# Kernel tuning notes

Hardware: AMD Instinct MI355X
Metric: run time of the kernel (lower is better)

## Reference

```python
import jax, jax.numpy as jnp
import numpy as np

B, S, D, F, E, TOP_K = 4, 2048, 1024, 4096, 8, 2


def setup_inputs() -> dict:
    key = jax.random.key(0)
    ks = jax.random.split(key, 6)
    sd = 1.0 / np.sqrt(D)
    sf = 1.0 / np.sqrt(F)
    return {
        "x": jax.random.normal(ks[0], (B, S, D), dtype=jnp.float32),
        "router_w": jax.random.normal(ks[1], (E, D), dtype=jnp.float32) * sd,
        "router_b": jnp.zeros((E,), dtype=jnp.float32),
        "w1": jax.random.normal(ks[2], (E, F, D), dtype=jnp.float32) * sd,  # Linear(d_model->d_ff) weight [out,in]
        "w2": jax.random.normal(ks[3], (E, D, F), dtype=jnp.float32) * sf,  # Linear(d_ff->d_model)
        "w3": jax.random.normal(ks[4], (E, F, D), dtype=jnp.float32) * sd,
    }


def reference(x, router_w, router_b, w1, w2, w3):
    # Router: softmax over experts, then top-k with renormalized gates.
    logits = jnp.einsum("bsd,ed->bse", x, router_w) + router_b          # [B,S,E]
    probs = jax.nn.softmax(logits, axis=-1)
    topk_p, topk_i = jax.lax.top_k(probs, TOP_K)                         # [B,S,K]
    topk_p = topk_p / jnp.sum(topk_p, axis=-1, keepdims=True)
    # Per-token combine weight for each expert (0 if not selected).
    combine = jnp.sum(jax.nn.one_hot(topk_i, E, dtype=x.dtype) * topk_p[..., None], axis=-2)  # [B,S,E]

    # Note: expert(x*mask)*mask == expert(x)*mask since SwiGLU(0)=0 (no bias).
    out = jnp.zeros_like(x)
    for e in range(E):  # small fixed expert count
        h = jax.nn.silu(jnp.einsum("bsd,fd->bsf", x, w1[e])) * jnp.einsum("bsd,fd->bsf", x, w3[e])
        out = out + combine[..., e:e + 1] * jnp.einsum("bsf,df->bsd", h, w2[e])
    return out
```

## Files before the change

kernel.cpp:

```cpp
#include <hip/hip_runtime.h>
#include <hip/hip_fp16.h>


#define NTOK 8192
#define D_ 1024
#define F_ 4096
#define E_ 8
#define SLOT_CAP 18432

using half8 = __attribute__((ext_vector_type(8))) _Float16;
using half4 = __attribute__((ext_vector_type(4))) _Float16;
using f32x4 = __attribute__((ext_vector_type(4))) float;

__device__ __forceinline__ void gload16(const void* g, void* l) {
  __builtin_amdgcn_global_load_lds((const __attribute__((address_space(1))) void*)g,
                                   (__attribute__((address_space(3))) void*)l, 16, 0, 0);
}

__global__ __launch_bounds__(256) void cvt_kernel(const float* __restrict__ src,
                                                  _Float16* __restrict__ dst, int n4) {
  int i = blockIdx.x * 256 + threadIdx.x;
  int stride = gridDim.x * 256;
  for (; i < n4; i += stride) {
    float4 v = ((const float4*)src)[i];
    half4 h;
    h.x = (_Float16)v.x; h.y = (_Float16)v.y; h.z = (_Float16)v.z; h.w = (_Float16)v.w;
    ((half4*)dst)[i] = h;
  }
}

__global__ __launch_bounds__(256) void cvt_w13_kernel(const float* __restrict__ w1,
                                                      const float* __restrict__ w3,
                                                      _Float16* __restrict__ w13, int n4) {
  int i = blockIdx.x * 256 + threadIdx.x;
  int stride = gridDim.x * 256;
  for (; i < n4; i += stride) {
    int d4 = i & 255;
    int row = i >> 8;
    int e = row >> 12, f = row & 4095;
    size_t vbase = ((size_t)e << 13) | ((size_t)(f >> 4) << 5) | (size_t)(f & 15);
    float4 v1 = ((const float4*)w1)[i];
    float4 v3 = ((const float4*)w3)[i];
    half4 h1, h3;
    h1.x = (_Float16)v1.x; h1.y = (_Float16)v1.y; h1.z = (_Float16)v1.z; h1.w = (_Float16)v1.w;
    h3.x = (_Float16)v3.x; h3.y = (_Float16)v3.y; h3.z = (_Float16)v3.z; h3.w = (_Float16)v3.w;
    ((half4*)w13)[vbase * 256 + d4] = h1;
    ((half4*)w13)[(vbase + 16) * 256 + d4] = h3;
  }
}

__global__ __launch_bounds__(256) void router_kernel(
    const float* __restrict__ x, const float* __restrict__ rw, const float* __restrict__ rbias,
    _Float16* __restrict__ x16, int* __restrict__ tok_e, float* __restrict__ tok_g,
    int* __restrict__ counts) {
  int wv = threadIdx.x >> 6, lane = threadIdx.x & 63;
  int t = blockIdx.x * 4 + wv;
  const float4* xr = (const float4*)(x + (size_t)t * D_);
  float acc[E_];
#pragma unroll
  for (int e = 0; e < E_; ++e) acc[e] = 0.f;
  for (int i = lane; i < D_ / 4; i += 64) {
    float4 xv = xr[i];
    half4 hx;
    hx.x = (_Float16)xv.x; hx.y = (_Float16)xv.y; hx.z = (_Float16)xv.z; hx.w = (_Float16)xv.w;
    ((half4*)(x16 + (size_t)t * D_))[i] = hx;
#pragma unroll
    for (int e = 0; e < E_; ++e) {
      float4 wv4 = ((const float4*)(rw + (size_t)e * D_))[i];
      acc[e] += xv.x * wv4.x + xv.y * wv4.y + xv.z * wv4.z + xv.w * wv4.w;
    }
  }
#pragma unroll
  for (int e = 0; e < E_; ++e) {
#pragma unroll
    for (int off = 32; off > 0; off >>= 1) acc[e] += __shfl_down(acc[e], off);
  }
  if (lane == 0) {
    float p[E_], mx = -1e30f;
#pragma unroll
    for (int e = 0; e < E_; ++e) { p[e] = acc[e] + rbias[e]; mx = fmaxf(mx, p[e]); }
#pragma unroll
    for (int e = 0; e < E_; ++e) p[e] = expf(p[e] - mx);
    int i0 = 0;
#pragma unroll
    for (int e = 1; e < E_; ++e) if (p[e] > p[i0]) i0 = e;
    int i1 = (i0 == 0) ? 1 : 0;
#pragma unroll
    for (int e = 0; e < E_; ++e) if (e != i0 && p[e] > p[i1]) i1 = e;
    float s = p[i0] + p[i1];
    tok_e[t * 2] = i0; tok_e[t * 2 + 1] = i1;
    tok_g[t * 2] = p[i0] / s; tok_g[t * 2 + 1] = p[i1] / s;
    atomicAdd(&counts[i0], 1); atomicAdd(&counts[i1], 1);
  }
}

__global__ void init_kernel(int* slot_token, int* counts, int* cursor) {
  int i = blockIdx.x * 256 + threadIdx.x;
  if (blockIdx.x == 0 && threadIdx.x < E_) { counts[threadIdx.x] = 0; cursor[threadIdx.x] = 0; }
  if (i < SLOT_CAP) slot_token[i] = 0;
}

__global__ void scan_kernel(const int* __restrict__ counts, int* __restrict__ offs) {
  if (threadIdx.x == 0) {
    int o = 0;
    for (int e = 0; e < E_; ++e) { offs[e] = o; o += ((counts[e] + 255) / 256) * 256; }
    offs[E_] = o;
  }
}

__global__ void scatter_kernel(const int* __restrict__ tok_e, const int* __restrict__ offs,
                               int* __restrict__ cursor, int* __restrict__ slot_token,
                               int* __restrict__ slot_of) {
  int i = blockIdx.x * 256 + threadIdx.x;
  if (i >= NTOK * 2) return;
  int e = tok_e[i];
  int pos = offs[e] + atomicAdd(&cursor[e], 1);
  slot_token[pos] = i >> 1;
  slot_of[i] = pos;
}

template <int BM, int MODE, int ORD, int MINW, int KD, int NBN, int RPX, int BEROWS>
__global__ __launch_bounds__(512, MINW) void moe_gemm_kernel(
    const _Float16* __restrict__ Amat, const _Float16* __restrict__ Bmat,
    const int* __restrict__ slot_token, const int* __restrict__ offs,
    void* __restrict__ outp) {
  constexpr int MROW = BM / 32;
  constexpr int AINS = BM / 128;
  constexpr int S = AINS + 2;
  constexpr int AH = BM * 32;
  constexpr int BUFH = (BM + 256) * 32;
  constexpr int NT = KD / 32;
  __shared__ _Float16 lds[3 * BUFH];

  int id = blockIdx.x;
  int xcd = id & 7, idx = id >> 3;
  int rb, nb;
  if constexpr (ORD == 0) {
    int band = idx / (8 * NBN);
    int i2 = idx - band * (8 * NBN);
    int rib = (RPX - band * 8) < 8 ? (RPX - band * 8) : 8;
    nb = i2 / rib;
    rb = xcd * RPX + band * 8 + (i2 - nb * rib);
  } else {
    nb = idx % NBN;
    rb = xcd * RPX + idx / NBN;
  }
  int row0 = rb * BM;
  if (row0 >= offs[E_]) return;
  int e = 0;
#pragma unroll
  for (int i = 1; i < E_; ++i) if (row0 >= offs[i]) e = i;

  int t = threadIdx.x, l = t & 63, w = t >> 6;
  int wr = w >> 2, wc = w & 3;
  int srow = t >> 2;
  int gsrc8 = ((l & 3) ^ ((l >> 3) & 3)) * 8;

  const _Float16* aSrc[AINS];
  if constexpr (MODE == 0) {
#pragma unroll
    for (int ins = 0; ins < AINS; ++ins) {
      int tk = slot_token[row0 + srow + ins * 128];
      aSrc[ins] = Amat + (size_t)tk * KD + gsrc8;
    }
  } else {
#pragma unroll
    for (int ins = 0; ins < AINS; ++ins)
      aSrc[ins] = Amat + (size_t)(row0 + srow + ins * 128) * KD + gsrc8;
  }
  const _Float16* bSrc0 = Bmat + ((size_t)e * BEROWS + (size_t)nb * 256 + srow) * KD + gsrc8;
  const _Float16* bSrc1 = bSrc0 + (size_t)128 * KD;

  auto stage = [&](int bi, int tt) {
#pragma unroll
    for (int ins = 0; ins < AINS; ++ins)
      gload16(aSrc[ins] + tt * 32, &lds[bi * BUFH + ins * 4096 + w * 512]);
    gload16(bSrc0 + tt * 32, &lds[bi * BUFH + AH + w * 512]);
    gload16(bSrc1 + tt * 32, &lds[bi * BUFH + AH + 4096 + w * 512]);
  };

  int fr = l & 15, kg = l >> 4;
  int swz8 = (kg ^ ((fr >> 1) & 3)) * 8;
  const int rA = (wr * (BM / 2) + fr) * 32 + swz8;
  const int rB = AH + (wc * 64 + fr) * 32 + swz8;
  auto ldA = [&](int bi, int mi) { return *(const half8*)&lds[bi * BUFH + rA + mi * 512]; };
  auto ldB = [&](int bi, int ni) { return *(const half8*)&lds[bi * BUFH + rB + ni * 512]; };

  f32x4 acc[MROW][4];
#pragma unroll
  for (int m = 0; m < MROW; ++m)
#pragma unroll
    for (int n = 0; n < 4; ++n) acc[m][n] = (f32x4){0.f, 0.f, 0.f, 0.f};

  stage(0, 0); stage(1, 1);
  asm volatile("s_waitcnt vmcnt(%0)" ::"i"(S) : "memory");
  __builtin_amdgcn_s_barrier();
  __builtin_amdgcn_sched_barrier(0);

  int b0 = 0, b1 = 1, b2 = 2;
  for (int j = 0; j < NT; ++j) {
    half8 a[MROW], b[4];
#pragma unroll
    for (int mi = 0; mi < MROW; ++mi) a[mi] = ldA(b0, mi);
#pragma unroll
    for (int ni = 0; ni < 4; ++ni) b[ni] = ldB(b0, ni);
    if (j + 2 < NT) stage(b2, j + 2);
    __builtin_amdgcn_s_setprio(1);
#pragma unroll
    for (int mi = 0; mi < MROW; ++mi)
#pragma unroll
      for (int ni = 0; ni < 4; ++ni)
        acc[mi][ni] = __builtin_amdgcn_mfma_f32_16x16x32_f16(a[mi], b[ni], acc[mi][ni], 0, 0, 0);
    __builtin_amdgcn_s_setprio(0);
    int ahead = NT - 1 - j;
    if (ahead >= 2)      asm volatile("s_waitcnt vmcnt(%0)" ::"i"(S) : "memory");
    else if (ahead == 1) asm volatile("s_waitcnt vmcnt(0)" ::: "memory");
    if (ahead >= 1) {
      __builtin_amdgcn_s_barrier();
      __builtin_amdgcn_sched_barrier(0);
    }
    int tmp = b0; b0 = b1; b1 = b2; b2 = tmp;
  }

  int q4 = kg * 4;
  if constexpr (MODE == 0) {
    _Float16* hb = (_Float16*)outp;
#pragma unroll
    for (int mi = 0; mi < MROW; ++mi) {
      size_t rbase = (size_t)(row0 + wr * (BM / 2) + mi * 16 + q4);
#pragma unroll
      for (int p = 0; p < 2; ++p) {
        int fc = nb * 128 + (wc * 2 + p) * 16 + fr;
#pragma unroll
        for (int i = 0; i < 4; ++i) {
          float gv = acc[mi][2 * p][i];
          float hv = gv / (1.f + __expf(-gv)) * acc[mi][2 * p + 1][i];
          hb[(rbase + i) * (size_t)F_ + fc] = (_Float16)hv;
        }
      }
    }
  } else {
    float* yb = (float*)outp;
#pragma unroll
    for (int mi = 0; mi < MROW; ++mi) {
      size_t rbase = (size_t)(row0 + wr * (BM / 2) + mi * 16 + q4);
#pragma unroll
      for (int ni = 0; ni < 4; ++ni) {
        int col = nb * 256 + wc * 64 + ni * 16 + fr;
#pragma unroll
        for (int i = 0; i < 4; ++i)
          yb[(rbase + i) * (size_t)D_ + col] = acc[mi][ni][i];
      }
    }
  }
}

__global__ __launch_bounds__(256) void combine_kernel(
    const float* __restrict__ ybuf, const int* __restrict__ slot_of,
    const float* __restrict__ tok_g, float* __restrict__ out) {
  int t = blockIdx.x, i = threadIdx.x;
  int s0 = slot_of[t * 2], s1 = slot_of[t * 2 + 1];
  float g0 = tok_g[t * 2], g1 = tok_g[t * 2 + 1];
  float4 a = ((const float4*)(ybuf + (size_t)s0 * D_))[i];
  float4 b = ((const float4*)(ybuf + (size_t)s1 * D_))[i];
  float4 r;
  r.x = g0 * a.x + g1 * b.x;
  r.y = g0 * a.y + g1 * b.y;
  r.z = g0 * a.z + g1 * b.z;
  r.w = g0 * a.w + g1 * b.w;
  ((float4*)(out + (size_t)t * D_))[i] = r;
}

extern "C" void kernel_launch(void* const* d_in, const int* in_sizes, int n_in,
                              void* d_out, int out_size, void* d_ws, size_t ws_size,
                              hipStream_t stream) {
  const float* x  = (const float*)d_in[0];
  const float* rw = (const float*)d_in[1];
  const float* rbc = (const float*)d_in[2];
  const float* w1 = (const float*)d_in[3];
  const float* w2 = (const float*)d_in[4];
  const float* w3 = (const float*)d_in[5];
  float* out = (float*)d_out;

  char* ws = (char*)d_ws;
  size_t off = 0;
  auto take = [&](size_t bytes) {
    char* p = ws + off;
    off = (off + bytes + 255) & ~(size_t)255;
    return p;
  };
  _Float16* x16 = (_Float16*)take((size_t)NTOK * D_ * 2);
  _Float16* w13 = (_Float16*)take((size_t)E_ * 2 * F_ * D_ * 2);
  _Float16* w2h = (_Float16*)take((size_t)E_ * D_ * F_ * 2);
  _Float16* hbuf = (_Float16*)take((size_t)SLOT_CAP * F_ * 2);
  float* ybuf = (float*)take((size_t)SLOT_CAP * D_ * 4);
  int* slot_token = (int*)take((size_t)SLOT_CAP * 4);
  int* tok_e = (int*)take((size_t)NTOK * 2 * 4);
  float* tok_g = (float*)take((size_t)NTOK * 2 * 4);
  int* slot_of = (int*)take((size_t)NTOK * 2 * 4);
  int* counts = (int*)take(E_ * 4);
  int* cursor = (int*)take(E_ * 4);
  int* offs = (int*)take((E_ + 1) * 4);

  cvt_w13_kernel<<<4096, 256, 0, stream>>>(w1, w3, w13, E_ * F_ * D_ / 4);
  cvt_kernel<<<4096, 256, 0, stream>>>(w2, w2h, E_ * D_ * F_ / 4);
  init_kernel<<<(SLOT_CAP + 255) / 256, 256, 0, stream>>>(slot_token, counts, cursor);
  router_kernel<<<NTOK / 4, 256, 0, stream>>>(x, rw, rbc, x16, tok_e, tok_g, counts);
  scan_kernel<<<1, 64, 0, stream>>>(counts, offs);
  scatter_kernel<<<(NTOK * 2 + 255) / 256, 256, 0, stream>>>(tok_e, offs, cursor, slot_token, slot_of);
  moe_gemm_kernel<256, 0, 0, 2, 1024, 32, 9, 8192><<<2304, 512, 0, stream>>>(
      x16, w13, slot_token, offs, (void*)hbuf);
  moe_gemm_kernel<128, 1, 1, 4, 4096, 4, 18, 1024><<<576, 512, 0, stream>>>(
      hbuf, w2h, slot_token, offs, (void*)ybuf);
  combine_kernel<<<NTOK, 256, 0, stream>>>(ybuf, slot_of, tok_g, out);
}
```

Baseline: 897.5 us.

## Use a four-buffer LDS ring with unrolled steps and 256-row tiles for down-projection

The GEMM mainloop moves to a four-stage LDS ring buffer. Each step issues its prefetch for step+2 before the LDS fragment reads, so loads into a buffer no longer wait on reads from the same buffer. The loop is unrolled by four so buffer indices are compile-time constants. The kernel is also fixed at BM=256, so the down-projection GEMM now uses 256-row tiles with half as many blocks. LDS use grows to 128KB per block, which allows only one block per CU, and the larger down-projection tiles may leave a partial second wave of blocks.

After: 917.2 us. +2.2%, slower.

```diff
diff --git a/kernel.cpp b/kernel.cpp
--- a/kernel.cpp
+++ b/kernel.cpp
@@ -119,18 +119,19 @@
   slot_of[i] = pos;
 }
 
-template <int BM, int MODE, int ORD, int MINW, int KD, int NBN, int RPX, int BEROWS>
-__global__ __launch_bounds__(512, MINW) void moe_gemm_kernel(
+template <int MODE, int ORD, int KD, int NBN, int RPX, int BEROWS>
+__global__ __launch_bounds__(512, 2) void moe_gemm_kernel(
     const _Float16* __restrict__ Amat, const _Float16* __restrict__ Bmat,
     const int* __restrict__ slot_token, const int* __restrict__ offs,
     void* __restrict__ outp) {
-  constexpr int MROW = BM / 32;
-  constexpr int AINS = BM / 128;
+  constexpr int BM = 256;
+  constexpr int MROW = 8;
+  constexpr int AINS = 2;
   constexpr int S = AINS + 2;
   constexpr int AH = BM * 32;
   constexpr int BUFH = (BM + 256) * 32;
   constexpr int NT = KD / 32;
-  __shared__ _Float16 lds[3 * BUFH];
+  __shared__ _Float16 lds[4 * BUFH];
 
   int id = blockIdx.x;
   int xcd = id & 7, idx = id >> 3;
@@ -156,35 +157,25 @@
   int srow = t >> 2;
   int gsrc8 = ((l & 3) ^ ((l >> 3) & 3)) * 8;
 
-  const _Float16* aSrc[AINS];
+  const _Float16* aP[AINS];
   if constexpr (MODE == 0) {
 #pragma unroll
     for (int ins = 0; ins < AINS; ++ins) {
       int tk = slot_token[row0 + srow + ins * 128];
-      aSrc[ins] = Amat + (size_t)tk * KD + gsrc8;
+      aP[ins] = Amat + (size_t)tk * KD + gsrc8;
     }
   } else {
 #pragma unroll
     for (int ins = 0; ins < AINS; ++ins)
-      aSrc[ins] = Amat + (size_t)(row0 + srow + ins * 128) * KD + gsrc8;
-  }
-  const _Float16* bSrc0 = Bmat + ((size_t)e * BEROWS + (size_t)nb * 256 + srow) * KD + gsrc8;
-  const _Float16* bSrc1 = bSrc0 + (size_t)128 * KD;
-
-  auto stage = [&](int bi, int tt) {
-#pragma unroll
-    for (int ins = 0; ins < AINS; ++ins)
-      gload16(aSrc[ins] + tt * 32, &lds[bi * BUFH + ins * 4096 + w * 512]);
-    gload16(bSrc0 + tt * 32, &lds[bi * BUFH + AH + w * 512]);
-    gload16(bSrc1 + tt * 32, &lds[bi * BUFH + AH + 4096 + w * 512]);
-  };
+      aP[ins] = Amat + (size_t)(row0 + srow + ins * 128) * KD + gsrc8;
+  }
+  const _Float16* b0P = Bmat + ((size_t)e * BEROWS + (size_t)nb * 256 + srow) * KD + gsrc8;
+  const _Float16* b1P = b0P + (size_t)128 * KD;
 
   int fr = l & 15, kg = l >> 4;
   int swz8 = (kg ^ ((fr >> 1) & 3)) * 8;
-  const int rA = (wr * (BM / 2) + fr) * 32 + swz8;
+  const int rA = (wr * 128 + fr) * 32 + swz8;
   const int rB = AH + (wc * 64 + fr) * 32 + swz8;
-  auto ldA = [&](int bi, int mi) { return *(const half8*)&lds[bi * BUFH + rA + mi * 512]; };
-  auto ldB = [&](int bi, int ni) { return *(const half8*)&lds[bi * BUFH + rB + ni * 512]; };
 
   f32x4 acc[MROW][4];
 #pragma unroll
@@ -192,42 +183,71 @@
 #pragma unroll
     for (int n = 0; n < 4; ++n) acc[m][n] = (f32x4){0.f, 0.f, 0.f, 0.f};
 
-  stage(0, 0); stage(1, 1);
+#pragma unroll
+  for (int ins = 0; ins < AINS; ++ins) gload16(aP[ins], &lds[ins * 4096 + w * 512]);
+  gload16(b0P, &lds[AH + w * 512]);
+  gload16(b1P, &lds[AH + 4096 + w * 512]);
+#pragma unroll
+  for (int ins = 0; ins < AINS; ++ins) gload16(aP[ins] + 32, &lds[BUFH + ins * 4096 + w * 512]);
+  gload16(b0P + 32, &lds[BUFH + AH + w * 512]);
+  gload16(b1P + 32, &lds[BUFH + AH + 4096 + w * 512]);
   asm volatile("s_waitcnt vmcnt(%0)" ::"i"(S) : "memory");
   __builtin_amdgcn_s_barrier();
   __builtin_amdgcn_sched_barrier(0);
 
-  int b0 = 0, b1 = 1, b2 = 2;
-  for (int j = 0; j < NT; ++j) {
-    half8 a[MROW], b[4];
-#pragma unroll
-    for (int mi = 0; mi < MROW; ++mi) a[mi] = ldA(b0, mi);
-#pragma unroll
-    for (int ni = 0; ni < 4; ++ni) b[ni] = ldB(b0, ni);
-    if (j + 2 < NT) stage(b2, j + 2);
-    __builtin_amdgcn_s_setprio(1);
-#pragma unroll
-    for (int mi = 0; mi < MROW; ++mi)
-#pragma unroll
-      for (int ni = 0; ni < 4; ++ni)
-        acc[mi][ni] = __builtin_amdgcn_mfma_f32_16x16x32_f16(a[mi], b[ni], acc[mi][ni], 0, 0, 0);
-    __builtin_amdgcn_s_setprio(0);
-    int ahead = NT - 1 - j;
-    if (ahead >= 2)      asm volatile("s_waitcnt vmcnt(%0)" ::"i"(S) : "memory");
-    else if (ahead == 1) asm volatile("s_waitcnt vmcnt(0)" ::: "memory");
-    if (ahead >= 1) {
-      __builtin_amdgcn_s_barrier();
-      __builtin_amdgcn_sched_barrier(0);
-    }
-    int tmp = b0; b0 = b1; b1 = b2; b2 = tmp;
-  }
+#pragma unroll
+  for (int ins = 0; ins < AINS; ++ins) aP[ins] += 64;
+  b0P += 64; b1P += 64;
+
+#define GEMM_STEP(U, PRE2, WN)                                                        \
+  {                                                                                   \
+    constexpr int bi_ = (U) & 3;                                                      \
+    constexpr int bs_ = ((U) + 2) & 3;                                                \
+    if (PRE2) {                                                                       \
+      _Pragma("unroll") for (int ins = 0; ins < AINS; ++ins)                          \
+          gload16(aP[ins] + (U) * 32, &lds[bs_ * BUFH + ins * 4096 + w * 512]);       \
+      gload16(b0P + (U) * 32, &lds[bs_ * BUFH + AH + w * 512]);                       \
+      gload16(b1P + (U) * 32, &lds[bs_ * BUFH + AH + 4096 + w * 512]);                \
+    }                                                                                 \
+    half8 a_[MROW], b_[4];                                                            \
+    _Pragma("unroll") for (int mi = 0; mi < MROW; ++mi)                               \
+        a_[mi] = *(const half8*)&lds[bi_ * BUFH + rA + mi * 512];                     \
+    _Pragma("unroll") for (int ni = 0; ni < 4; ++ni)                                  \
+        b_[ni] = *(const half8*)&lds[bi_ * BUFH + rB + ni * 512];                     \
+    __builtin_amdgcn_s_setprio(1);                                                    \
+    _Pragma("unroll") for (int mi = 0; mi < MROW; ++mi)                               \
+        _Pragma("unroll") for (int ni = 0; ni < 4; ++ni)                              \
+            acc[mi][ni] = __builtin_amdgcn_mfma_f32_16x16x32_f16(a_[mi], b_[ni],      \
+                                                                 acc[mi][ni], 0, 0, 0); \
+    __builtin_amdgcn_s_setprio(0);                                                    \
+    if ((WN) >= 0) {                                                                  \
+      asm volatile("s_waitcnt vmcnt(%0)" ::"i"((WN) >= 0 ? (WN) : 0) : "memory");     \
+      __builtin_amdgcn_s_barrier();                                                   \
+      __builtin_amdgcn_sched_barrier(0);                                              \
+    }                                                                                 \
+  }
+
+  for (int j4 = 0; j4 < NT - 4; j4 += 4) {
+    GEMM_STEP(0, true, S)
+    GEMM_STEP(1, true, S)
+    GEMM_STEP(2, true, S)
+    GEMM_STEP(3, true, S)
+#pragma unroll
+    for (int ins = 0; ins < AINS; ++ins) aP[ins] += 128;
+    b0P += 128; b1P += 128;
+  }
+  GEMM_STEP(0, true, S)
+  GEMM_STEP(1, true, S)
+  GEMM_STEP(2, false, 0)
+  GEMM_STEP(3, false, -1)
+#undef GEMM_STEP
 
   int q4 = kg * 4;
   if constexpr (MODE == 0) {
     _Float16* hb = (_Float16*)outp;
 #pragma unroll
     for (int mi = 0; mi < MROW; ++mi) {
-      size_t rbase = (size_t)(row0 + wr * (BM / 2) + mi * 16 + q4);
+      size_t rbase = (size_t)(row0 + wr * 128 + mi * 16 + q4);
 #pragma unroll
       for (int p = 0; p < 2; ++p) {
         int fc = nb * 128 + (wc * 2 + p) * 16 + fr;
@@ -243,7 +263,7 @@
     float* yb = (float*)outp;
 #pragma unroll
     for (int mi = 0; mi < MROW; ++mi) {
-      size_t rbase = (size_t)(row0 + wr * (BM / 2) + mi * 16 + q4);
+      size_t rbase = (size_t)(row0 + wr * 128 + mi * 16 + q4);
 #pragma unroll
       for (int ni = 0; ni < 4; ++ni) {
         int col = nb * 256 + wc * 64 + ni * 16 + fr;
@@ -308,9 +328,9 @@
   router_kernel<<<NTOK / 4, 256, 0, stream>>>(x, rw, rbc, x16, tok_e, tok_g, counts);
   scan_kernel<<<1, 64, 0, stream>>>(counts, offs);
   scatter_kernel<<<(NTOK * 2 + 255) / 256, 256, 0, stream>>>(tok_e, offs, cursor, slot_token, slot_of);
-  moe_gemm_kernel<256, 0, 0, 2, 1024, 32, 9, 8192><<<2304, 512, 0, stream>>>(
+  moe_gemm_kernel<0, 0, 1024, 32, 9, 8192><<<2304, 512, 0, stream>>>(
       x16, w13, slot_token, offs, (void*)hbuf);
-  moe_gemm_kernel<128, 1, 1, 4, 4096, 4, 18, 1024><<<576, 512, 0, stream>>>(
+  moe_gemm_kernel<1, 1, 4096, 4, 9, 1024><<<288, 512, 0, stream>>>(
       hbuf, w2h, slot_token, offs, (void*)ybuf);
   combine_kernel<<<NTOK, 256, 0, stream>>>(ybuf, slot_of, tok_g, out);
 }
```
